# Optimization experiments

Hardware: AMD Instinct MI355X
Metric: run time of the kernel (lower is better)

## Reference

```python
import jax, jax.numpy as jnp
import numpy as np
from jax.scipy.linalg import block_diag

N_STATE, N_INPUT, HORIZON = 32, 16, 64


def setup_inputs() -> dict:
    key = jax.random.key(0)
    kA, kB, kC, kx = jax.random.split(key, 4)
    n_all = N_STATE + N_INPUT
    A = jax.random.normal(kA, (N_STATE, N_STATE), dtype=jnp.float32)
    B = jax.random.normal(kB, (N_STATE, N_INPUT), dtype=jnp.float32)
    Craw = jax.random.normal(kC, (HORIZON, n_all, n_all), dtype=jnp.float32)
    # symmetric positive-definite stage costs -> nonsingular KKT system
    C = jnp.einsum('tij,tkj->tik', Craw, Craw) / jnp.sqrt(jnp.float32(n_all)) \
        + jnp.eye(n_all, dtype=jnp.float32)
    x0 = jax.random.normal(kx, (N_STATE,), dtype=jnp.float32)
    return {"A": A, "B": B, "C": C, "T": HORIZON, "x0": x0}


def reference(A, B, C, T, x0):
    n_state = A.shape[0]
    n_input = B.shape[1]
    n_all = n_state + n_input
    dt = A.dtype

    # cost_mat: block-diagonal [n_all*T, n_all*T]
    cost_mat = block_diag(*C)

    # dynamics: [n_state*T, n_all*T]
    AB = jnp.concatenate((A, B), axis=1)              # [n_state, n_all]
    AB_blk = block_diag(*([AB] * (T - 1)))            # [(T-1)*n_state, (T-1)*n_all]
    dynamics = jnp.zeros((n_state * T, n_all * T), dtype=dt)
    dynamics = dynamics.at[:n_state, :n_state].set(jnp.eye(n_state, dtype=dt))
    dynamics = dynamics.at[n_state:n_state + (T - 1) * n_state,
                           :(T - 1) * n_all].set(AB_blk)
    # -I coupling entries: row n_state*t + i, col n_all*t + i, t=1..T-1
    t = jnp.arange(1, T)
    rows = (n_state * t)[:, None] + jnp.arange(n_state)[None, :]
    cols = (n_all * t)[:, None] + jnp.arange(n_state)[None, :]
    dynamics = dynamics.at[rows, cols].set(jnp.asarray(-1.0, dt))

    zero_mat = jnp.zeros((n_state * T, n_state * T), dtype=dt)
    full_mat = jnp.block([[cost_mat, dynamics.T],
                          [dynamics, zero_mat]])      # [(n_all+n_state)*T]^2

    # rhs: zeros except x0 at the start of the dynamics block
    sol = jnp.zeros(n_all * T + n_state * T, dtype=dt)
    sol = sol.at[n_all * T: n_all * T + n_state].set(x0)

    tau_mu = jnp.linalg.solve(full_mat, sol[:, None])[:, 0]
    tau_star = tau_mu[:n_all * T]
    mu_star = tau_mu[n_all * T:]
    return tau_star, mu_star
```

## Files before the change

### kernel.cpp

```cpp
#include <hip/hip_runtime.h>


namespace {

constexpr int NS  = 32;
constexpr int NI  = 16;
constexpr int NA  = 48;
constexpr int TT  = 64;
constexpr int NTH = 256;
constexpr int NBLK = 64;

__device__ __forceinline__ void fma4(float4& a, float s, const float4& b) {
  a.x += s * b.x; a.y += s * b.y; a.z += s * b.z; a.w += s * b.w;
}
__device__ __forceinline__ void fms4(float4& a, float s, const float4& b) {
  a.x -= s * b.x; a.y -= s * b.y; a.z -= s * b.z; a.w -= s * b.w;
}
__device__ __forceinline__ float dot4(const float4& a, const float4& b) {
  return a.x * b.x + a.y * b.y + a.z * b.z + a.w * b.w;
}
__device__ __forceinline__ float rdlane(float v, int l) {
  return __int_as_float(__builtin_amdgcn_readlane(__float_as_int(v), l));
}

template<int K>
__device__ __forceinline__ void tile_outer(const float* Acol0, int lda,
                                           const float* Bcol0, int ldb,
                                           float4 acc[4]) {
  #pragma unroll
  for (int m = 0; m < K; ++m) {
    const float4 va = *(const float4*)(Acol0 + m * lda);
    const float4 vb = *(const float4*)(Bcol0 + m * ldb);
    fma4(acc[0], va.x, vb); fma4(acc[1], va.y, vb);
    fma4(acc[2], va.z, vb); fma4(acc[3], va.w, vb);
  }
}

template<int KQ>
__device__ __forceinline__ void tile_dot(const float* Arow0, int lda,
                                         const float* Brow0, int ldb,
                                         float acc[4][4]) {
  #pragma unroll
  for (int q = 0; q < KQ; ++q) {
    float4 va[4], vb[4];
    #pragma unroll
    for (int r = 0; r < 4; ++r) va[r] = *(const float4*)(Arow0 + r * lda + 4 * q);
    #pragma unroll
    for (int c = 0; c < 4; ++c) vb[c] = *(const float4*)(Brow0 + c * ldb + 4 * q);
    #pragma unroll
    for (int r = 0; r < 4; ++r)
      #pragma unroll
      for (int c = 0; c < 4; ++c) acc[r][c] += dot4(va[r], vb[c]);
  }
}

__device__ __forceinline__ void gbar(unsigned* flags, unsigned* gen, unsigned p) {
  __syncthreads();
  if (threadIdx.x == 0) {
    __threadfence();
    __hip_atomic_store(&flags[blockIdx.x], p, __ATOMIC_RELAXED,
                       __HIP_MEMORY_SCOPE_AGENT);
  }
  if (blockIdx.x == 0) {
    if (threadIdx.x < NBLK) {
      while (__hip_atomic_load(&flags[threadIdx.x], __ATOMIC_RELAXED,
                               __HIP_MEMORY_SCOPE_AGENT) < p)
        __builtin_amdgcn_s_sleep(1);
    }
    __syncthreads();
    if (threadIdx.x == 0)
      __hip_atomic_store(gen, p, __ATOMIC_RELAXED, __HIP_MEMORY_SCOPE_AGENT);
  } else if (threadIdx.x == 0) {
    while (__hip_atomic_load(gen, __ATOMIC_RELAXED,
                             __HIP_MEMORY_SCOPE_AGENT) < p)
      __builtin_amdgcn_s_sleep(1);
  }
  if (threadIdx.x == 0) __threadfence();
  __syncthreads();
}

__device__ __forceinline__ float step_dot(const float4 m[8], float x) {
  float a0 = 0.f, a1 = 0.f, a2 = 0.f, a3 = 0.f;
  #pragma unroll
  for (int q = 0; q < 8; ++q) {
    a0 += rdlane(x, 4 * q + 0) * m[q].x;
    a1 += rdlane(x, 4 * q + 1) * m[q].y;
    a2 += rdlane(x, 4 * q + 2) * m[q].z;
    a3 += rdlane(x, 4 * q + 3) * m[q].w;
  }
  return (a0 + a1) + (a2 + a3);
}

__global__ __launch_bounds__(NTH, 1) void lqr_all(
    const float* __restrict__ A, const float* __restrict__ Bm,
    const float* __restrict__ C, const float* __restrict__ x0,
    float* __restrict__ out,
    float* __restrict__ Sb0, float* __restrict__ Sb1,
    float* __restrict__ Kall, float* __restrict__ Mall,
    float* __restrict__ xs, unsigned* __restrict__ bar) {
  __shared__ float sC [NA][NA];
  __shared__ float sAB[NS][NA];
  __shared__ float sRi[NI][NI];
  __shared__ float sRiST[NS][NI];
  __shared__ float sBRi [NS][NI];
  __shared__ float sAi[NS][NS], sCi[NS][NS], sJi[NS][NS];
  __shared__ float sAj[NS][NS], sCj[NS][NS], sJj[NS][NS], sAjT[NS][NS];
  __shared__ float sT1[NS][NS], sT1T[NS][NS];
  __shared__ float sY1[NS][NS], sY2[NS][NS], sY3T[NS][NS], sW[NS][NS];
  __shared__ float sX[NS][NS], sZm[NS][NS];
  __shared__ float sP[NS][NS], sG[NS][NA], sFu[NI][NA], sK[NI][NS];

  const int t = blockIdx.x, tid = threadIdx.x, lane = tid & 63, wid = tid >> 6;
  unsigned* flags = bar;
  unsigned* gen   = bar + 64;
  unsigned p = 1;

  {
    const float* Ct = C + (size_t)t * NA * NA;
    for (int e = tid; e < NA * NA; e += NTH) sC[e / NA][e % NA] = Ct[e];
    for (int e = tid; e < NS * NA; e += NTH) {
      int i = e / NA, j = e % NA;
      sAB[i][j] = (j < NS) ? A[i * NS + j] : Bm[i * NI + (j - NS)];
    }
    __syncthreads();
    if (wid == 0 && lane < 32) {
      const int c = lane;
      float f[NI];
      #pragma unroll
      for (int i = 0; i < NI; ++i)
        f[i] = (c < NI) ? sC[NS + i][NS + c] : ((c - NI) == i ? 1.f : 0.f);
      #pragma unroll
      for (int k = 0; k < NI; ++k) {
        float mi[NI];
        #pragma unroll
        for (int i = 0; i < NI; ++i) mi[i] = rdlane(f[i], k);
        const float inv = 1.0f / mi[k];
        f[k] *= inv;
        #pragma unroll
        for (int i = 0; i < NI; ++i) if (i != k) f[i] -= mi[i] * f[k];
      }
      if (c >= NI) {
        #pragma unroll
        for (int i = 0; i < NI; ++i) sRi[i][c - NI] = f[i];
      }
    }
    __syncthreads();
    if (tid < 32) {
      const int a = tid >> 2, b = tid & 3;
      float acc[4][4];
      #pragma unroll
      for (int r = 0; r < 4; ++r)
        #pragma unroll
        for (int c = 0; c < 4; ++c) acc[r][c] = 0.f;
      tile_dot<4>(&sC[4 * a][NS], NA, &sRi[4 * b][0], NI, acc);
      #pragma unroll
      for (int r = 0; r < 4; ++r)
        *(float4*)&sRiST[4 * a + r][4 * b] =
            make_float4(acc[r][0], acc[r][1], acc[r][2], acc[r][3]);
    } else if (tid < 64) {
      const int q = tid - 32, a = q >> 2, b = q & 3;
      float acc[4][4];
      #pragma unroll
      for (int r = 0; r < 4; ++r)
        #pragma unroll
        for (int c = 0; c < 4; ++c) acc[r][c] = 0.f;
      tile_dot<4>(&sAB[4 * a][NS], NA, &sRi[4 * b][0], NI, acc);
      #pragma unroll
      for (int r = 0; r < 4; ++r)
        *(float4*)&sBRi[4 * a + r][4 * b] =
            make_float4(acc[r][0], acc[r][1], acc[r][2], acc[r][3]);
    }
    __syncthreads();
    float* outA = Sb0 + (size_t)t * 3072;
    float* outC = outA + 1024;
    float* outJ = outA + 2048;
    if (tid < 64) {
      const int a = tid >> 3, b = tid & 7;
      float acc[4][4];
      #pragma unroll
      for (int r = 0; r < 4; ++r)
        #pragma unroll
        for (int c = 0; c < 4; ++c) acc[r][c] = 0.f;
      tile_dot<4>(&sRiST[4 * a][0], NI, &sC[4 * b][NS], NA, acc);
      #pragma unroll
      for (int r = 0; r < 4; ++r) {
        const float4 q4 = *(const float4*)&sC[4 * a + r][4 * b];
        *(float4*)(outJ + (4 * a + r) * NS + 4 * b) =
            make_float4(q4.x - acc[r][0], q4.y - acc[r][1],
                        q4.z - acc[r][2], q4.w - acc[r][3]);
      }
    } else if (tid < 128) {
      const int q = tid - 64, a = q >> 3, b = q & 7;
      float acc[4][4];
      #pragma unroll
      for (int r = 0; r < 4; ++r)
        #pragma unroll
        for (int c = 0; c < 4; ++c) acc[r][c] = 0.f;
      tile_dot<4>(&sBRi[4 * a][0], NI, &sC[4 * b][NS], NA, acc);
      #pragma unroll
      for (int r = 0; r < 4; ++r) {
        const float4 a4 = *(const float4*)&sAB[4 * a + r][4 * b];
        *(float4*)(outA + (4 * a + r) * NS + 4 * b) =
            make_float4(a4.x - acc[r][0], a4.y - acc[r][1],
                        a4.z - acc[r][2], a4.w - acc[r][3]);
      }
    } else if (tid < 192) {
      const int q = tid - 128, a = q >> 3, b = q & 7;
      float acc[4][4];
      #pragma unroll
      for (int r = 0; r < 4; ++r)
        #pragma unroll
        for (int c = 0; c < 4; ++c) acc[r][c] = 0.f;
      tile_dot<4>(&sBRi[4 * a][0], NI, &sAB[4 * b][NS], NA, acc);
      #pragma unroll
      for (int r = 0; r < 4; ++r)
        *(float4*)(outC + (4 * a + r) * NS + 4 * b) =
            make_float4(acc[r][0], acc[r][1], acc[r][2], acc[r][3]);
    }
  }
  gbar(flags, gen, p++);

  for (int l = 0; l < 6; ++l) {
    const int off = 1 << l;
    const float* Sin = (l & 1) ? Sb1 : Sb0;
    float* Sout = (l & 1) ? Sb0 : Sb1;
    const float* Ei = Sin + (size_t)t * 3072;
    float* Eo = Sout + (size_t)t * 3072;
    if (t + off >= TT) {
      const float4* src = (const float4*)Ei;
      float4* dst = (float4*)Eo;
      #pragma unroll
      for (int r = 0; r < 3; ++r) dst[tid + 256 * r] = src[tid + 256 * r];
    } else {
      const float* Ej = Sin + (size_t)(t + off) * 3072;
      {
        const float4* a4 = (const float4*)Ei;
        ((float4*)sAi)[tid] = a4[tid];
        ((float4*)sCi)[tid] = a4[256 + tid];
        ((float4*)sJi)[tid] = a4[512 + tid];
        const float4* b4 = (const float4*)Ej;
        ((float4*)sAj)[tid] = b4[tid];
        ((float4*)sCj)[tid] = b4[256 + tid];
        ((float4*)sJj)[tid] = b4[512 + tid];
      }
      __syncthreads();
      #pragma unroll
      for (int r = 0; r < 4; ++r) {
        const int e = tid + 256 * r, i = e >> 5, j = e & 31;
        sAjT[j][i] = sAj[i][j];
      }
      if (tid < 64) {
        const int a = tid >> 3, b = tid & 7;
        float4 acc[4] = {make_float4(0,0,0,0), make_float4(0,0,0,0),
                         make_float4(0,0,0,0), make_float4(0,0,0,0)};
        tile_outer<NS>(&sCi[0][4 * a], NS, &sJj[0][4 * b], NS, acc);
        if (a == b) { acc[0].x += 1.f; acc[1].y += 1.f; acc[2].z += 1.f; acc[3].w += 1.f; }
        #pragma unroll
        for (int r = 0; r < 4; ++r) *(float4*)&sX[4 * a + r][4 * b] = acc[r];
      }
      __syncthreads();
      if (wid == 0) {
        const int c = lane;
        float f[NS];
        #pragma unroll
        for (int i = 0; i < NS; ++i)
          f[i] = (c < NS) ? sX[i][c] : ((c - NS) == i ? 1.f : 0.f);
        #pragma unroll
        for (int k = 0; k < NS; ++k) {
          float mi[NS];
          #pragma unroll
          for (int i = 0; i < NS; ++i) mi[i] = rdlane(f[i], k);
          const float inv = 1.0f / mi[k];
          f[k] *= inv;
          #pragma unroll
          for (int i = 0; i < NS; ++i) if (i != k) f[i] -= mi[i] * f[k];
        }
        if (c >= NS) {
          const int col = c - NS;
          #pragma unroll
          for (int i = 0; i < NS; ++i) sT1[i][col] = f[i];
          #pragma unroll
          for (int q = 0; q < 8; ++q)
            *(float4*)&sT1T[col][4 * q] =
                make_float4(f[4 * q], f[4 * q + 1], f[4 * q + 2], f[4 * q + 3]);
        }
      }
      __syncthreads();
      if (tid < 192) {
        const int grp = tid >> 6, q = tid & 63, a = q >> 3, b = q & 7;
        float4 acc[4] = {make_float4(0,0,0,0), make_float4(0,0,0,0),
                         make_float4(0,0,0,0), make_float4(0,0,0,0)};
        if (grp == 0) {
          tile_outer<NS>(&sT1T[0][4 * a], NS, &sAi[0][4 * b], NS, acc);
          #pragma unroll
          for (int r = 0; r < 4; ++r) *(float4*)&sY1[4 * a + r][4 * b] = acc[r];
        } else if (grp == 1) {
          tile_outer<NS>(&sT1T[0][4 * a], NS, &sCi[0][4 * b], NS, acc);
          #pragma unroll
          for (int r = 0; r < 4; ++r) *(float4*)&sY2[4 * a + r][4 * b] = acc[r];
        } else {
          tile_outer<NS>(&sT1[0][4 * a], NS, &sJj[0][4 * b], NS, acc);
          #pragma unroll
          for (int r = 0; r < 4; ++r) *(float4*)&sY3T[4 * a + r][4 * b] = acc[r];
        }
      }
      __syncthreads();
      if (tid < 192) {
        const int grp = tid >> 6, q = tid & 63, a = q >> 3, b = q & 7;
        float4 acc[4] = {make_float4(0,0,0,0), make_float4(0,0,0,0),
                         make_float4(0,0,0,0), make_float4(0,0,0,0)};
        if (grp == 0) {
          tile_outer<NS>(&sAjT[0][4 * a], NS, &sY1[0][4 * b], NS, acc);
          #pragma unroll
          for (int r = 0; r < 4; ++r) *(float4*)&sX[4 * a + r][4 * b] = acc[r];
        } else if (grp == 1) {
          tile_outer<NS>(&sAjT[0][4 * a], NS, &sY2[0][4 * b], NS, acc);
          #pragma unroll
          for (int r = 0; r < 4; ++r) *(float4*)&sZm[4 * a + r][4 * b] = acc[r];
        } else {
          tile_outer<NS>(&sY3T[0][4 * a], NS, &sAi[0][4 * b], NS, acc);
          #pragma unroll
          for (int r = 0; r < 4; ++r) *(float4*)&sW[4 * a + r][4 * b] = acc[r];
        }
      }
      __syncthreads();
      if (tid < 64) {
        const int a = tid >> 3, b = tid & 7;
        float acc[4][4];
        #pragma unroll
        for (int r = 0; r < 4; ++r)
          #pragma unroll
          for (int c = 0; c < 4; ++c) acc[r][c] = 0.f;
        tile_dot<8>(&sZm[4 * a][0], NS, &sAj[4 * b][0], NS, acc);
        #pragma unroll
        for (int r = 0; r < 4; ++r) {
          const float4 c4 = *(const float4*)&sCj[4 * a + r][4 * b];
          *(float4*)&sY2[4 * a + r][4 * b] =
              make_float4(acc[r][0] + c4.x, acc[r][1] + c4.y,
                          acc[r][2] + c4.z, acc[r][3] + c4.w);
        }
      } else if (tid < 128) {
        const int q = tid - 64, a = q >> 3, b = q & 7;
        float4 acc[4] = {make_float4(0,0,0,0), make_float4(0,0,0,0),
                         make_float4(0,0,0,0), make_float4(0,0,0,0)};
        tile_outer<NS>(&sAi[0][4 * a], NS, &sW[0][4 * b], NS, acc);
        #pragma unroll
        for (int r = 0; r < 4; ++r) {
          const float4 j4 = *(const float4*)&sJi[4 * a + r][4 * b];
          acc[r].x += j4.x; acc[r].y += j4.y; acc[r].z += j4.z; acc[r].w += j4.w;
          *(float4*)&sY1[4 * a + r][4 * b] = acc[r];
        }
      }
      __syncthreads();
      {
        float4* o = (float4*)Eo;
        o[tid]       = ((const float4*)sX)[tid];
        o[256 + tid] = ((const float4*)sY2)[tid];
        o[512 + tid] = ((const float4*)sY1)[tid];
      }
    }
    gbar(flags, gen, p++);
  }

  {
    for (int e = tid; e < NS * NA; e += NTH) {
      int i = e / NA, j = e % NA;
      sAB[i][j] = (j < NS) ? A[i * NS + j] : Bm[i * NI + (j - NS)];
    }
    if (t == TT - 1) {
      ((float4*)sP)[tid] = make_float4(0.f, 0.f, 0.f, 0.f);
    } else {
      const float4* j4 = (const float4*)(Sb0 + (size_t)(t + 1) * 3072 + 2048);
      ((float4*)sP)[tid] = j4[tid];
    }
    const int ui = tid / 12, uk = tid - 12 * ui;
    float4 cr0 = make_float4(0,0,0,0), cr1 = make_float4(0,0,0,0);
    float4 cr2 = make_float4(0,0,0,0), cr3 = make_float4(0,0,0,0);
    if (tid < 48) {
      const float* Ct = C + (size_t)t * NA * NA;
      cr0 = *(const float4*)&Ct[(NS + 4 * ui + 0) * NA + 4 * uk];
      cr1 = *(const float4*)&Ct[(NS + 4 * ui + 1) * NA + 4 * uk];
      cr2 = *(const float4*)&Ct[(NS + 4 * ui + 2) * NA + 4 * uk];
      cr3 = *(const float4*)&Ct[(NS + 4 * ui + 3) * NA + 4 * uk];
    }
    __syncthreads();
    if (tid < 96) {
      const int gi = tid / 12, gk = tid - 12 * gi;
      float4 acc[4] = {make_float4(0,0,0,0), make_float4(0,0,0,0),
                       make_float4(0,0,0,0), make_float4(0,0,0,0)};
      tile_outer<NS>(&sP[0][4 * gi], NS, &sAB[0][4 * gk], NA, acc);
      #pragma unroll
      for (int r = 0; r < 4; ++r) *(float4*)&sG[4 * gi + r][4 * gk] = acc[r];
    }
    __syncthreads();
    if (tid < 48) {
      float4 acc[4] = {cr0, cr1, cr2, cr3};
      tile_outer<NS>(&sAB[0][NS + 4 * ui], NA, &sG[0][4 * uk], NA, acc);
      #pragma unroll
      for (int r = 0; r < 4; ++r) *(float4*)&sFu[4 * ui + r][4 * uk] = acc[r];
    }
    __syncthreads();
    if (wid == 0) {
      const int col = (lane < 16) ? (NS + lane) : (lane - 16);
      float f[NI];
      #pragma unroll
      for (int i = 0; i < NI; ++i) f[i] = sFu[i][col];
      #pragma unroll
      for (int k = 0; k < NI; ++k) {
        float mi[NI];
        #pragma unroll
        for (int i = 0; i < NI; ++i) mi[i] = rdlane(f[i], k);
        const float inv = 1.0f / mi[k];
        f[k] *= inv;
        #pragma unroll
        for (int i = 0; i < NI; ++i) if (i != k) f[i] -= mi[i] * f[k];
      }
      if (lane >= 16 && lane < 48) {
        const int b = lane - 16;
        #pragma unroll
        for (int i = 0; i < NI; ++i) {
          sK[i][b] = f[i];
          Kall[(size_t)t * NI * NS + i * NS + b] = f[i];
        }
      }
    }
    __syncthreads();
    if (tid < 64) {
      const int ma = tid >> 3, mb = tid & 7;
      float4 a0 = *(const float4*)&sAB[4 * ma + 0][4 * mb];
      float4 a1 = *(const float4*)&sAB[4 * ma + 1][4 * mb];
      float4 a2 = *(const float4*)&sAB[4 * ma + 2][4 * mb];
      float4 a3 = *(const float4*)&sAB[4 * ma + 3][4 * mb];
      #pragma unroll
      for (int q = 0; q < 4; ++q) {
        const float4 vf0 = *(const float4*)&sAB[4 * ma + 0][NS + 4 * q];
        const float4 vf1 = *(const float4*)&sAB[4 * ma + 1][NS + 4 * q];
        const float4 vf2 = *(const float4*)&sAB[4 * ma + 2][NS + 4 * q];
        const float4 vf3 = *(const float4*)&sAB[4 * ma + 3][NS + 4 * q];
        #pragma unroll
        for (int d = 0; d < 4; ++d) {
          const float4 vkk = *(const float4*)&sK[4 * q + d][4 * mb];
          const float s0 = (d == 0) ? vf0.x : (d == 1) ? vf0.y : (d == 2) ? vf0.z : vf0.w;
          const float s1 = (d == 0) ? vf1.x : (d == 1) ? vf1.y : (d == 2) ? vf1.z : vf1.w;
          const float s2 = (d == 0) ? vf2.x : (d == 1) ? vf2.y : (d == 2) ? vf2.z : vf2.w;
          const float s3 = (d == 0) ? vf3.x : (d == 1) ? vf3.y : (d == 2) ? vf3.z : vf3.w;
          fms4(a0, s0, vkk); fms4(a1, s1, vkk); fms4(a2, s2, vkk); fms4(a3, s3, vkk);
        }
      }
      float4* Mt = (float4*)(Mall + (size_t)t * NS * NS);
      Mt[(4 * ma + 0) * 8 + mb] = a0;
      Mt[(4 * ma + 1) * 8 + mb] = a1;
      Mt[(4 * ma + 2) * 8 + mb] = a2;
      Mt[(4 * ma + 3) * 8 + mb] = a3;
    }
  }
  gbar(flags, gen, p++);

  if (t == 0 && wid == 0) {
    const int i = lane;
    if (i < NS) {
      const float4* Mg = (const float4*)Mall;
      float4 mA[8], mB[8];
      float x = x0[i];
      out[i] = x; xs[i] = x;
      #pragma unroll
      for (int q = 0; q < 8; ++q) mA[q] = Mg[0 * 256 + i * 8 + q];
      #pragma unroll
      for (int q = 0; q < 8; ++q) mB[q] = Mg[1 * 256 + i * 8 + q];
      for (int s = 0; s < TT - 1; s += 2) {
        x = step_dot(mA, x);
        out[(s + 1) * NA + i] = x; xs[(s + 1) * NS + i] = x;
        if (s + 2 < TT - 1) {
          #pragma unroll
          for (int q = 0; q < 8; ++q) mA[q] = Mg[(s + 2) * 256 + i * 8 + q];
        }
        if (s + 1 < TT - 1) {
          x = step_dot(mB, x);
          out[(s + 2) * NA + i] = x; xs[(s + 2) * NS + i] = x;
          if (s + 3 < TT - 1) {
            #pragma unroll
            for (int q = 0; q < 8; ++q) mB[q] = Mg[(s + 3) * 256 + i * 8 + q];
          }
        }
      }
    }
  }
  gbar(flags, gen, p++);

  {
    const float4* xr = (const float4*)(xs + (size_t)t * NS);
    if (tid < NI) {
      const float4* Kr = (const float4*)(Kall + (size_t)t * NI * NS + tid * NS);
      float acc = 0.f;
      #pragma unroll
      for (int q = 0; q < 8; ++q) acc += dot4(Kr[q], xr[q]);
      out[t * NA + NS + tid] = -acc;
    } else if (tid < NI + NS) {
      const int i = tid - NI;
      const float4* Pr = (const float4*)(Sb0 + (size_t)t * 3072 + 2048 + i * NS);
      float acc = 0.f;
      #pragma unroll
      for (int q = 0; q < 8; ++q) acc += dot4(Pr[q], xr[q]);
      out[NA * TT + t * NS + i] = (t == 0) ? -acc : acc;
    }
  }
}

}

extern "C" void kernel_launch(void* const* d_in, const int* in_sizes, int n_in,
                              void* d_out, int out_size, void* d_ws, size_t ws_size,
                              hipStream_t stream) {
  const float* A  = (const float*)d_in[0];
  const float* Bm = (const float*)d_in[1];
  const float* C  = (const float*)d_in[2];
  const float* x0 = (const float*)d_in[4];
  float* out = (float*)d_out;

  float* Sb0  = (float*)d_ws;
  float* Sb1  = Sb0 + (size_t)TT * 3072;
  float* Kall = Sb1 + (size_t)TT * 3072;
  float* Mall = Kall + (size_t)TT * NI * NS;
  float* xs   = Mall + (size_t)TT * NS * NS;
  unsigned* bar = (unsigned*)(xs + (size_t)TT * NS);

  hipMemsetAsync(bar, 0, 128 * sizeof(unsigned), stream);
  hipLaunchKernelGGL(lqr_all, dim3(NBLK), dim3(NTH), 0, stream,
                     A, Bm, C, x0, out, Sb0, Sb1, Kall, Mall, xs, bar);
}
```

Measured before the change: 148.9 us.

## Replace centralized grid barrier with all-to-all flag barrier and fence-free atomic exchange

```diff
diff --git a/kernel.cpp b/kernel.cpp
--- a/kernel.cpp
+++ b/kernel.cpp
@@ -10,6 +10,8 @@
 constexpr int NTH = 256;
 constexpr int NBLK = 64;
 
+using ull = unsigned long long;
+
 __device__ __forceinline__ void fma4(float4& a, float s, const float4& b) {
   a.x += s * b.x; a.y += s * b.y; a.z += s * b.z; a.w += s * b.w;
 }
@@ -21,6 +23,36 @@
 }
 __device__ __forceinline__ float rdlane(float v, int l) {
   return __int_as_float(__builtin_amdgcn_readlane(__float_as_int(v), l));
+}
+
+__device__ __forceinline__ ull ald(const ull* p) {
+  return __hip_atomic_load(p, __ATOMIC_RELAXED, __HIP_MEMORY_SCOPE_AGENT);
+}
+__device__ __forceinline__ void ast(ull* p, ull v) {
+  __hip_atomic_store(p, v, __ATOMIC_RELAXED, __HIP_MEMORY_SCOPE_AGENT);
+}
+__device__ __forceinline__ float aldf(const float* p) {
+  return __uint_as_float(__hip_atomic_load((const unsigned*)p,
+      __ATOMIC_RELAXED, __HIP_MEMORY_SCOPE_AGENT));
+}
+__device__ __forceinline__ void astf(float* p, float v) {
+  __hip_atomic_store((unsigned*)p, __float_as_uint(v),
+      __ATOMIC_RELAXED, __HIP_MEMORY_SCOPE_AGENT);
+}
+__device__ __forceinline__ ull pack2(float x, float y) {
+  return (ull)__float_as_uint(x) | ((ull)__float_as_uint(y) << 32);
+}
+__device__ __forceinline__ float2 unpack2(ull v) {
+  return make_float2(__uint_as_float((unsigned)v),
+                     __uint_as_float((unsigned)(v >> 32)));
+}
+__device__ __forceinline__ float4 ald4(const ull* p) {
+  ull lo = ald(p), hi = ald(p + 1);
+  float2 a = unpack2(lo), b = unpack2(hi);
+  return make_float4(a.x, a.y, b.x, b.y);
+}
+__device__ __forceinline__ void ast4(ull* p, const float4& v) {
+  ast(p, pack2(v.x, v.y)); ast(p + 1, pack2(v.z, v.w));
 }
 
 template<int K>
@@ -54,28 +86,17 @@
   }
 }
 
-__device__ __forceinline__ void gbar(unsigned* flags, unsigned* gen, unsigned p) {
+__device__ __forceinline__ void gbar(unsigned* flags, unsigned p) {
+  asm volatile("s_waitcnt vmcnt(0)" ::: "memory");
   __syncthreads();
-  if (threadIdx.x == 0) {
-    __threadfence();
+  if (threadIdx.x == 0)
     __hip_atomic_store(&flags[blockIdx.x], p, __ATOMIC_RELAXED,
                        __HIP_MEMORY_SCOPE_AGENT);
-  }
-  if (blockIdx.x == 0) {
-    if (threadIdx.x < NBLK) {
-      while (__hip_atomic_load(&flags[threadIdx.x], __ATOMIC_RELAXED,
-                               __HIP_MEMORY_SCOPE_AGENT) < p)
-        __builtin_amdgcn_s_sleep(1);
-    }
-    __syncthreads();
-    if (threadIdx.x == 0)
-      __hip_atomic_store(gen, p, __ATOMIC_RELAXED, __HIP_MEMORY_SCOPE_AGENT);
-  } else if (threadIdx.x == 0) {
-    while (__hip_atomic_load(gen, __ATOMIC_RELAXED,
+  if (threadIdx.x < NBLK) {
+    while (__hip_atomic_load(&flags[threadIdx.x], __ATOMIC_RELAXED,
                              __HIP_MEMORY_SCOPE_AGENT) < p)
       __builtin_amdgcn_s_sleep(1);
   }
-  if (threadIdx.x == 0) __threadfence();
   __syncthreads();
 }
 
@@ -97,7 +118,7 @@
     float* __restrict__ out,
     float* __restrict__ Sb0, float* __restrict__ Sb1,
     float* __restrict__ Kall, float* __restrict__ Mall,
-    float* __restrict__ xs, unsigned* __restrict__ bar) {
+    float* __restrict__ xs, unsigned* __restrict__ flags) {
   __shared__ float sC [NA][NA];
   __shared__ float sAB[NS][NA];
   __shared__ float sRi[NI][NI];
@@ -109,10 +130,9 @@
   __shared__ float sY1[NS][NS], sY2[NS][NS], sY3T[NS][NS], sW[NS][NS];
   __shared__ float sX[NS][NS], sZm[NS][NS];
   __shared__ float sP[NS][NS], sG[NS][NA], sFu[NI][NA], sK[NI][NS];
+  __shared__ float sXt[NS];
 
   const int t = blockIdx.x, tid = threadIdx.x, lane = tid & 63, wid = tid >> 6;
-  unsigned* flags = bar;
-  unsigned* gen   = bar + 64;
   unsigned p = 1;
 
   {
@@ -171,9 +191,9 @@
             make_float4(acc[r][0], acc[r][1], acc[r][2], acc[r][3]);
     }
     __syncthreads();
-    float* outA = Sb0 + (size_t)t * 3072;
-    float* outC = outA + 1024;
-    float* outJ = outA + 2048;
+    ull* outA = (ull*)(Sb0 + (size_t)t * 3072);
+    ull* outC = outA + 512;
+    ull* outJ = outA + 1024;
     if (tid < 64) {
       const int a = tid >> 3, b = tid & 7;
       float acc[4][4];
@@ -185,9 +205,10 @@
       #pragma unroll
       for (int r = 0; r < 4; ++r) {
         const float4 q4 = *(const float4*)&sC[4 * a + r][4 * b];
-        *(float4*)(outJ + (4 * a + r) * NS + 4 * b) =
-            make_float4(q4.x - acc[r][0], q4.y - acc[r][1],
-                        q4.z - acc[r][2], q4.w - acc[r][3]);
+        const float4 v = make_float4(q4.x - acc[r][0], q4.y - acc[r][1],
+                                     q4.z - acc[r][2], q4.w - acc[r][3]);
+        *(float4*)&sJi[4 * a + r][4 * b] = v;
+        ast4(outJ + ((4 * a + r) * NS + 4 * b) / 2, v);
       }
     } else if (tid < 128) {
       const int q = tid - 64, a = q >> 3, b = q & 7;
@@ -200,9 +221,10 @@
       #pragma unroll
       for (int r = 0; r < 4; ++r) {
         const float4 a4 = *(const float4*)&sAB[4 * a + r][4 * b];
-        *(float4*)(outA + (4 * a + r) * NS + 4 * b) =
-            make_float4(a4.x - acc[r][0], a4.y - acc[r][1],
-                        a4.z - acc[r][2], a4.w - acc[r][3]);
+        const float4 v = make_float4(a4.x - acc[r][0], a4.y - acc[r][1],
+                                     a4.z - acc[r][2], a4.w - acc[r][3]);
+        *(float4*)&sAi[4 * a + r][4 * b] = v;
+        ast4(outA + ((4 * a + r) * NS + 4 * b) / 2, v);
       }
     } else if (tid < 192) {
       const int q = tid - 128, a = q >> 3, b = q & 7;
@@ -213,35 +235,36 @@
         for (int c = 0; c < 4; ++c) acc[r][c] = 0.f;
       tile_dot<4>(&sBRi[4 * a][0], NI, &sAB[4 * b][NS], NA, acc);
       #pragma unroll
-      for (int r = 0; r < 4; ++r)
-        *(float4*)(outC + (4 * a + r) * NS + 4 * b) =
-            make_float4(acc[r][0], acc[r][1], acc[r][2], acc[r][3]);
-    }
-  }
-  gbar(flags, gen, p++);
+      for (int r = 0; r < 4; ++r) {
+        const float4 v = make_float4(acc[r][0], acc[r][1], acc[r][2], acc[r][3]);
+        *(float4*)&sCi[4 * a + r][4 * b] = v;
+        ast4(outC + ((4 * a + r) * NS + 4 * b) / 2, v);
+      }
+    }
+  }
+  gbar(flags, p++);
 
   for (int l = 0; l < 6; ++l) {
     const int off = 1 << l;
     const float* Sin = (l & 1) ? Sb1 : Sb0;
     float* Sout = (l & 1) ? Sb0 : Sb1;
-    const float* Ei = Sin + (size_t)t * 3072;
-    float* Eo = Sout + (size_t)t * 3072;
+    ull* Eo = (ull*)(Sout + (size_t)t * 3072);
     if (t + off >= TT) {
-      const float4* src = (const float4*)Ei;
-      float4* dst = (float4*)Eo;
-      #pragma unroll
-      for (int r = 0; r < 3; ++r) dst[tid + 256 * r] = src[tid + 256 * r];
+      ast(Eo + tid,        ((const ull*)sAi)[tid]);
+      ast(Eo + 256 + tid,  ((const ull*)sAi)[tid + 256]);
+      ast(Eo + 512 + tid,  ((const ull*)sCi)[tid]);
+      ast(Eo + 768 + tid,  ((const ull*)sCi)[tid + 256]);
+      ast(Eo + 1024 + tid, ((const ull*)sJi)[tid]);
+      ast(Eo + 1280 + tid, ((const ull*)sJi)[tid + 256]);
     } else {
-      const float* Ej = Sin + (size_t)(t + off) * 3072;
+      const ull* Ej = (const ull*)(Sin + (size_t)(t + off) * 3072);
       {
-        const float4* a4 = (const float4*)Ei;
-        ((float4*)sAi)[tid] = a4[tid];
-        ((float4*)sCi)[tid] = a4[256 + tid];
-        ((float4*)sJi)[tid] = a4[512 + tid];
-        const float4* b4 = (const float4*)Ej;
-        ((float4*)sAj)[tid] = b4[tid];
-        ((float4*)sCj)[tid] = b4[256 + tid];
-        ((float4*)sJj)[tid] = b4[512 + tid];
+        ull r0 = ald(Ej + tid),        r1 = ald(Ej + 256 + tid);
+        ull r2 = ald(Ej + 512 + tid),  r3 = ald(Ej + 768 + tid);
+        ull r4 = ald(Ej + 1024 + tid), r5 = ald(Ej + 1280 + tid);
+        ((ull*)sAj)[tid] = r0; ((ull*)sAj)[tid + 256] = r1;
+        ((ull*)sCj)[tid] = r2; ((ull*)sCj)[tid + 256] = r3;
+        ((ull*)sJj)[tid] = r4; ((ull*)sJj)[tid + 256] = r5;
       }
       __syncthreads();
       #pragma unroll
@@ -353,13 +376,18 @@
       }
       __syncthreads();
       {
-        float4* o = (float4*)Eo;
-        o[tid]       = ((const float4*)sX)[tid];
-        o[256 + tid] = ((const float4*)sY2)[tid];
-        o[512 + tid] = ((const float4*)sY1)[tid];
-      }
-    }
-    gbar(flags, gen, p++);
+        ull x0_ = ((const ull*)sX)[tid],  x1_ = ((const ull*)sX)[tid + 256];
+        ull y0_ = ((const ull*)sY2)[tid], y1_ = ((const ull*)sY2)[tid + 256];
+        ull z0_ = ((const ull*)sY1)[tid], z1_ = ((const ull*)sY1)[tid + 256];
+        ast(Eo + tid, x0_);        ast(Eo + 256 + tid, x1_);
+        ast(Eo + 512 + tid, y0_);  ast(Eo + 768 + tid, y1_);
+        ast(Eo + 1024 + tid, z0_); ast(Eo + 1280 + tid, z1_);
+        ((ull*)sAi)[tid] = x0_; ((ull*)sAi)[tid + 256] = x1_;
+        ((ull*)sCi)[tid] = y0_; ((ull*)sCi)[tid + 256] = y1_;
+        ((ull*)sJi)[tid] = z0_; ((ull*)sJi)[tid + 256] = z1_;
+      }
+    }
+    gbar(flags, p++);
   }
 
   {
@@ -370,8 +398,9 @@
     if (t == TT - 1) {
       ((float4*)sP)[tid] = make_float4(0.f, 0.f, 0.f, 0.f);
     } else {
-      const float4* j4 = (const float4*)(Sb0 + (size_t)(t + 1) * 3072 + 2048);
-      ((float4*)sP)[tid] = j4[tid];
+      const ull* j64 = (const ull*)(Sb0 + (size_t)(t + 1) * 3072) + 1024;
+      ((ull*)sP)[tid] = ald(j64 + tid);
+      ((ull*)sP)[tid + 256] = ald(j64 + 256 + tid);
     }
     const int ui = tid / 12, uk = tid - 12 * ui;
     float4 cr0 = make_float4(0,0,0,0), cr1 = make_float4(0,0,0,0);
@@ -420,7 +449,7 @@
         #pragma unroll
         for (int i = 0; i < NI; ++i) {
           sK[i][b] = f[i];
-          Kall[(size_t)t * NI * NS + i * NS + b] = f[i];
+          astf(&Kall[(size_t)t * NI * NS + i * NS + b], f[i]);
         }
       }
     }
@@ -447,60 +476,67 @@
           fms4(a0, s0, vkk); fms4(a1, s1, vkk); fms4(a2, s2, vkk); fms4(a3, s3, vkk);
         }
       }
-      float4* Mt = (float4*)(Mall + (size_t)t * NS * NS);
-      Mt[(4 * ma + 0) * 8 + mb] = a0;
-      Mt[(4 * ma + 1) * 8 + mb] = a1;
-      Mt[(4 * ma + 2) * 8 + mb] = a2;
-      Mt[(4 * ma + 3) * 8 + mb] = a3;
-    }
-  }
-  gbar(flags, gen, p++);
+      ull* Mt = (ull*)(Mall + (size_t)t * NS * NS);
+      ast4(Mt + (4 * ma + 0) * 16 + 2 * mb, a0);
+      ast4(Mt + (4 * ma + 1) * 16 + 2 * mb, a1);
+      ast4(Mt + (4 * ma + 2) * 16 + 2 * mb, a2);
+      ast4(Mt + (4 * ma + 3) * 16 + 2 * mb, a3);
+    }
+  }
+  gbar(flags, p++);
 
   if (t == 0 && wid == 0) {
     const int i = lane;
     if (i < NS) {
-      const float4* Mg = (const float4*)Mall;
+      const ull* Mg = (const ull*)Mall;
       float4 mA[8], mB[8];
       float x = x0[i];
-      out[i] = x; xs[i] = x;
-      #pragma unroll
-      for (int q = 0; q < 8; ++q) mA[q] = Mg[0 * 256 + i * 8 + q];
-      #pragma unroll
-      for (int q = 0; q < 8; ++q) mB[q] = Mg[1 * 256 + i * 8 + q];
+      out[i] = x; astf(&xs[i], x);
+      #pragma unroll
+      for (int q = 0; q < 8; ++q) mA[q] = ald4(Mg + 0 * 512 + i * 16 + 2 * q);
+      #pragma unroll
+      for (int q = 0; q < 8; ++q) mB[q] = ald4(Mg + 1 * 512 + i * 16 + 2 * q);
       for (int s = 0; s < TT - 1; s += 2) {
         x = step_dot(mA, x);
-        out[(s + 1) * NA + i] = x; xs[(s + 1) * NS + i] = x;
+        out[(s + 1) * NA + i] = x; astf(&xs[(s + 1) * NS + i], x);
         if (s + 2 < TT - 1) {
           #pragma unroll
-          for (int q = 0; q < 8; ++q) mA[q] = Mg[(s + 2) * 256 + i * 8 + q];
+          for (int q = 0; q < 8; ++q) mA[q] = ald4(Mg + (s + 2) * 512 + i * 16 + 2 * q);
         }
         if (s + 1 < TT - 1) {
           x = step_dot(mB, x);
-          out[(s + 2) * NA + i] = x; xs[(s + 2) * NS + i] = x;
+          out[(s + 2) * NA + i] = x; astf(&xs[(s + 2) * NS + i], x);
           if (s + 3 < TT - 1) {
             #pragma unroll
-            for (int q = 0; q < 8; ++q) mB[q] = Mg[(s + 3) * 256 + i * 8 + q];
+            for (int q = 0; q < 8; ++q) mB[q] = ald4(Mg + (s + 3) * 512 + i * 16 + 2 * q);
           }
         }
       }
     }
   }
-  gbar(flags, gen, p++);
+  gbar(flags, p++);
 
   {
-    const float4* xr = (const float4*)(xs + (size_t)t * NS);
+    if (tid < NS) sXt[tid] = aldf(&xs[(size_t)t * NS + tid]);
+    __syncthreads();
     if (tid < NI) {
-      const float4* Kr = (const float4*)(Kall + (size_t)t * NI * NS + tid * NS);
+      const ull* Kr = (const ull*)(Kall + (size_t)t * NI * NS + tid * NS);
       float acc = 0.f;
       #pragma unroll
-      for (int q = 0; q < 8; ++q) acc += dot4(Kr[q], xr[q]);
+      for (int k = 0; k < 16; ++k) {
+        float2 v = unpack2(ald(Kr + k));
+        acc += v.x * sXt[2 * k] + v.y * sXt[2 * k + 1];
+      }
       out[t * NA + NS + tid] = -acc;
     } else if (tid < NI + NS) {
       const int i = tid - NI;
-      const float4* Pr = (const float4*)(Sb0 + (size_t)t * 3072 + 2048 + i * NS);
+      const ull* Pr = (const ull*)(Sb0 + (size_t)t * 3072 + 2048 + i * NS);
       float acc = 0.f;
       #pragma unroll
-      for (int q = 0; q < 8; ++q) acc += dot4(Pr[q], xr[q]);
+      for (int k = 0; k < 16; ++k) {
+        float2 v = unpack2(ald(Pr + k));
+        acc += v.x * sXt[2 * k] + v.y * sXt[2 * k + 1];
+      }
       out[NA * TT + t * NS + i] = (t == 0) ? -acc : acc;
     }
   }
@@ -522,9 +558,9 @@
   float* Kall = Sb1 + (size_t)TT * 3072;
   float* Mall = Kall + (size_t)TT * NI * NS;
   float* xs   = Mall + (size_t)TT * NS * NS;
-  unsigned* bar = (unsigned*)(xs + (size_t)TT * NS);
-
-  hipMemsetAsync(bar, 0, 128 * sizeof(unsigned), stream);
+  unsigned* flags = (unsigned*)(xs + (size_t)TT * NS);
+
+  hipMemsetAsync(flags, 0, 128 * sizeof(unsigned), stream);
   hipLaunchKernelGGL(lqr_all, dim3(NBLK), dim3(NTH), 0, stream,
-                     A, Bm, C, x0, out, Sb0, Sb1, Kall, Mall, xs, bar);
-}
+                     A, Bm, C, x0, out, Sb0, Sb1, Kall, Mall, xs, flags);
+}
```

Measured after the change: 155.3 us. 1.04x slower.
